# Kernel tuning notes

Hardware: AMD Instinct MI355X
Metric: run time of the kernel (lower is better)

## Reference

```python
import jax, jax.numpy as jnp
import numpy as np

K = 100
TEMPERATURE = 0.1


def setup_inputs() -> dict:
    key = jax.random.key(0)
    k1, k2 = jax.random.split(key)
    x = jax.random.normal(k1, (8, 128, 60, 60), dtype=jnp.float32)
    W = jax.random.normal(k2, (128, 2 * K), dtype=jnp.float32) * 0.02  # torch Linear(k*2, d_model).weight
    b = jnp.zeros((128,), dtype=jnp.float32)
    return {"x": x, "W": W, "b": b}


def reference(x, W, b):
    x0, x1 = jnp.split(x, 2, axis=0)
    n, c, h, w = x0.shape
    hw = h * w
    # n c h w -> n (h w) c
    f0 = jnp.transpose(x0.reshape(n, c, hw), (0, 2, 1))
    f1 = jnp.transpose(x1.reshape(n, c, hw), (0, 2, 1))
    # (f0/sqrt(c)) @ (f1/sqrt(c))^T / T  ==  f0 @ f1^T / (c*T)
    sm = jnp.einsum('nld,nsd->nls', f0, f1) / (c * TEMPERATURE)
    cm = (jax.nn.softmax(sm, axis=1) * jax.nn.softmax(sm, axis=2)).reshape(n, hw * hw)
    _, topi = jax.lax.top_k(cm, K)  # (n, K)
    qindex = topi // hw
    rindex = topi % hw
    coords0 = jnp.stack([qindex % w, qindex // w], axis=-1).astype(jnp.float32) / w  # (n, K, 2) as (x, y)
    coords1 = jnp.stack([rindex % w, rindex // w], axis=-1).astype(jnp.float32) / w
    # create_meshgrid(h, w, normalized=False): (1, h*w, 2) with (x, y), row-major
    gy, gx = jnp.meshgrid(jnp.arange(h), jnp.arange(w), indexing='ij')
    grid = jnp.stack([gx, gy], axis=-1).reshape(1, hw, 2).astype(jnp.float32) / w
    offsets0 = grid[:, :, None, :] - coords0[:, None, :, :]  # (n, hw, K, 2)
    offsets1 = grid[:, :, None, :] - coords1[:, None, :, :]
    emb0 = offsets0.reshape(n, hw, 2 * K) @ W.T + b  # (n, hw, d_model)
    emb1 = offsets1.reshape(n, hw, 2 * K) @ W.T + b
    f0 = f0 + emb0
    f1 = f1 + emb1
    f = jnp.concatenate([f0, f1], axis=0)  # (2n, hw, d)
    # n (h w) d -> n d h w
    return jnp.transpose(f, (0, 2, 1)).reshape(2 * n, c, h, w)
```

## Files before the change

kernel.cpp:

```cpp
#include <hip/hip_runtime.h>

#define HW 3600
#define PADR 3712
#define NF4 900
#define CAP 16384
#define KSEL 100
#define NT 58
typedef unsigned long long U64;

using short8   = __attribute__((ext_vector_type(8))) short;
using float4v  = __attribute__((ext_vector_type(4))) float;
using float16v = __attribute__((ext_vector_type(16))) float;

__device__ __forceinline__ unsigned monof(float f) {
    unsigned b = __float_as_uint(f);
    return (b & 0x80000000u) ? ~b : (b | 0x80000000u);
}
__device__ __forceinline__ float unmonof(unsigned m) {
    return __uint_as_float((m & 0x80000000u) ? (m ^ 0x80000000u) : ~m);
}
__device__ __forceinline__ unsigned short f2bf(float f) {
    unsigned b = __float_as_uint(f);
    return (unsigned short)((b + 0x7FFFu + ((b >> 16) & 1u)) >> 16);
}
__device__ __forceinline__ float bf2f(unsigned short h) {
    return __uint_as_float(((unsigned)h) << 16);
}
__device__ __forceinline__ void async16(const void* g, void* l) {
    __builtin_amdgcn_global_load_lds((const __attribute__((address_space(1))) void*)g,
                                     (__attribute__((address_space(3))) void*)l, 16, 0, 0);
}


__global__ __launch_bounds__(256) void conv_k(
    const float* __restrict__ x,
    unsigned short* __restrict__ hiT, unsigned short* __restrict__ loT,
    unsigned* __restrict__ zero_region)
{
    int b = blockIdx.z, l0 = blockIdx.x * 64, d0 = blockIdx.y * 64;
    __shared__ float t[64][65];
    int tid = threadIdx.x;
    if (blockIdx.y == 0 && blockIdx.z == 0) {
        int base = blockIdx.x * 512;
        for (int i = tid; i < 512; i += 256) {
            int g = base + i;
            if (g < 28808) zero_region[g] = 0u;
        }
    }
#pragma unroll
    for (int r = 0; r < 4; r++) {
        int idx = tid + 256 * r;
        int d = idx >> 4, lq = idx & 15;
        int l = l0 + lq * 4;
        const float* src = x + ((size_t)b * 128 + d0 + d) * HW;
        float4 v;
        if (l + 3 < HW) v = *(const float4*)(src + l);
        else {
            v.x = (l     < HW) ? src[l]     : 0.f;
            v.y = (l + 1 < HW) ? src[l + 1] : 0.f;
            v.z = (l + 2 < HW) ? src[l + 2] : 0.f;
            v.w = (l + 3 < HW) ? src[l + 3] : 0.f;
        }
        t[lq * 4 + 0][d] = v.x; t[lq * 4 + 1][d] = v.y;
        t[lq * 4 + 2][d] = v.z; t[lq * 4 + 3][d] = v.w;
    }
    __syncthreads();
    const int rblk = l0 >> 7;
#pragma unroll
    for (int r = 0; r < 2; r++) {
        int idx = tid + 256 * r;
        int l = idx & 63, dq = idx >> 6;
        unsigned hp[4], lp[4];
#pragma unroll
        for (int j = 0; j < 4; j++) {
            float f0 = t[l][dq * 8 + 2 * j], f1 = t[l][dq * 8 + 2 * j + 1];
            unsigned short h0 = f2bf(f0), h1 = f2bf(f1);
            unsigned short g0 = f2bf(f0 - bf2f(h0)), g1 = f2bf(f1 - bf2f(h1));
            hp[j] = (unsigned)h0 | ((unsigned)h1 << 16);
            lp[j] = (unsigned)g0 | ((unsigned)g1 << 16);
        }
        size_t o = ((size_t)(b * 29 + rblk) * 16 + (d0 >> 3) + dq) * 1024
                 + (size_t)((l0 + l) & 127) * 8;
        *(uint4*)(hiT + o) = make_uint4(hp[0], hp[1], hp[2], hp[3]);
        *(uint4*)(loT + o) = make_uint4(lp[0], lp[1], lp[2], lp[3]);
    }
}

__global__ __launch_bounds__(512) void gemm_mfma_k(
    const unsigned short* __restrict__ hiT, const unsigned short* __restrict__ loT,
    float* __restrict__ den_row, float* __restrict__ den_col,
    float* __restrict__ maxvt)
{
    const int batch = blockIdx.z, bx = blockIdx.x, by = blockIdx.y;
    __shared__ __align__(16) union SU {
        unsigned short st[4][4][128][8];
        float T[8192];
    } u;
    __shared__ float rsB[128];
    __shared__ float csB[128];
    __shared__ unsigned mxB[2][128];

    const int tid = threadIdx.x;
    const int lane = tid & 63, w = tid >> 6;
    const int l31 = lane & 31, h = lane >> 5;
    const int p = w >> 1, halfr = w & 1;
    const int rg = w >> 2, cg = w & 3;

    if (tid < 128) { rsB[tid] = 0.f; csB[tid] = 0.f; }
    if (tid < 256) mxB[tid >> 7][tid & 127] = 0u;

    const unsigned short* psrc = (p == 0) ? hiT : (p == 1) ? loT : (p == 2) ? hiT : loT;
    const int bsel = (p < 2) ? batch : batch + 4;
    const int rblk = (p < 2) ? by : bx;
    const size_t cbase = ((size_t)(bsel * 29 + rblk) * 16) * 1024;

    float16v acc[2];
    acc[0] = (float16v)(0.f);
    acc[1] = (float16v)(0.f);

    for (int k0 = 0; k0 < 128; k0 += 32) {
#pragma unroll
        for (int kb = 0; kb < 4; kb++) {
            const unsigned short* g = psrc + cbase + (size_t)((k0 >> 3) + kb) * 1024
                                    + (halfr << 9) + lane * 8;
            async16(g, &u.st[p][kb][halfr << 6][0]);
        }
        __syncthreads();
#pragma unroll
        for (int j = 0; j < 2; j++) {
            int kb = j * 2 + h;
            short8 ah[2], al[2], bh, bl;
            ah[0] = *(const short8*)&u.st[0][kb][rg * 64 + l31][0];
            ah[1] = *(const short8*)&u.st[0][kb][rg * 64 + 32 + l31][0];
            al[0] = *(const short8*)&u.st[1][kb][rg * 64 + l31][0];
            al[1] = *(const short8*)&u.st[1][kb][rg * 64 + 32 + l31][0];
            bh    = *(const short8*)&u.st[2][kb][cg * 32 + l31][0];
            bl    = *(const short8*)&u.st[3][kb][cg * 32 + l31][0];
#pragma unroll
            for (int mt = 0; mt < 2; mt++) {
                acc[mt] = __builtin_amdgcn_mfma_f32_32x32x16_bf16(ah[mt], bh, acc[mt], 0, 0, 0);
                acc[mt] = __builtin_amdgcn_mfma_f32_32x32x16_bf16(ah[mt], bl, acc[mt], 0, 0, 0);
                acc[mt] = __builtin_amdgcn_mfma_f32_32x32x16_bf16(al[mt], bh, acc[mt], 0, 0, 0);
            }
        }
        __syncthreads();
    }

    const float scale = 0.078125f;
    float* T = u.T + w * 1024;
    const bool interior = (bx < 28) && (by < 28);
    const int col0 = bx * 128 + cg * 32 + l31;
    const bool cv = interior || (col0 < HW);
    float cs = 0.f;

#pragma unroll
    for (int mt = 0; mt < 2; mt++) {
#pragma unroll
        for (int reg = 0; reg < 16; reg++) {
            float v = acc[mt][reg] * scale;
            float e = cv ? __expf(v) : 0.f;
            int rloc = (reg & 3) + 8 * (reg >> 2) + 4 * h;
            bool rv = interior || (by * 128 + rg * 64 + mt * 32 + rloc < HW);
            if (rv) cs += e;
            T[rloc * 32 + (l31 ^ rloc)] = e;
        }
        __asm__ __volatile__("s_waitcnt lgkmcnt(0)" ::: "memory");
        {
            float ps = 0.f, pm = 0.f;
#pragma unroll
            for (int i = 0; i < 16; i++) {
                float tv_ = T[l31 * 32 + ((h * 16 + i) ^ l31)];
                ps += tv_;
                pm = fmaxf(pm, tv_);
            }
            ps += __shfl_xor(ps, 32);
            pm = fmaxf(pm, __shfl_xor(pm, 32));
            if (h == 0) {
                atomicAdd(&rsB[rg * 64 + mt * 32 + l31], ps);
                atomicMax(&mxB[cg >> 1][rg * 64 + mt * 32 + l31],
                          monof(__logf(pm)));
            }
        }
        __asm__ __volatile__("s_waitcnt lgkmcnt(0)" ::: "memory");
    }
    cs += __shfl_xor(cs, 32);
    if (h == 0) atomicAdd(&csB[cg * 32 + l31], cs);
    __syncthreads();

    if (tid < 128) {
        int l = by * 128 + tid;
        if (l < HW) atomicAdd(&den_row[(size_t)batch * HW + l], rsB[tid]);
        int s = bx * 128 + tid;
        if (s < HW) atomicAdd(&den_col[(size_t)batch * HW + s], csB[tid]);
    }
    if (tid < 256) {
        int tile = tid >> 7, row = tid & 127;
        int l = by * 128 + row;
        if (l < HW)
            maxvt[((size_t)batch * NT + bx * 2 + tile) * PADR + l] =
                unmonof(mxB[tile][row]);
    }
}

__global__ __launch_bounds__(256) void stat_k(
    const float* __restrict__ den_row, const float* __restrict__ den_col,
    const float* __restrict__ maxvt, float* __restrict__ keylb)
{
    const int b = blockIdx.z, tid = threadIdx.x;
    __shared__ float lncS[HW];
    __shared__ float mlsS[NT];
    for (int i = tid; i < HW; i += 256)
        lncS[i] = __logf(den_col[(size_t)b * HW + i]);
    __syncthreads();
    if (tid < NT) {
        float mx = -3.4e38f;
        int s0 = tid * 64, s1 = s0 + 64; if (s1 > HW) s1 = HW;
        for (int s = s0; s < s1; s++) mx = fmaxf(mx, lncS[s]);
        mlsS[tid] = (s0 < HW) ? mx : 1e30f;
    }
    __syncthreads();
    int j = blockIdx.x * 240 + tid;
    if (tid < 240 && j < HW) {
        const float* mvb = maxvt + (size_t)b * NT * PADR;
        float b0 = -3.4e38f, b1_ = -3.4e38f;
#pragma unroll 4
        for (int tt = 0; tt < 58; tt += 2) {
            b0  = fmaxf(b0,  2.0f * mvb[(size_t)tt * PADR + j]       - mlsS[tt]);
            b1_ = fmaxf(b1_, 2.0f * mvb[(size_t)(tt + 1) * PADR + j] - mlsS[tt + 1]);
        }
        keylb[(size_t)b * HW + j] = fmaxf(b0, b1_) - __logf(den_row[(size_t)b * HW + j]);
    }
}

__global__ __launch_bounds__(256) void tau_k(
    const float* __restrict__ keylb, float* __restrict__ tau)
{
    const int b = blockIdx.z, tid = threadIdx.x;
    __shared__ unsigned keyS[HW];
    __shared__ unsigned hist[4096];
    __shared__ unsigned hpc[256];
    __shared__ int b1S, c1S, b2S, lcnt;
    __shared__ unsigned bestS;
    __shared__ unsigned list[1024];

    for (int i = tid; i < 4096; i += 256) hist[i] = 0u;
    if (tid == 0) { lcnt = 0; bestS = 0u; }
    __syncthreads();
    for (int i = tid; i < HW; i += 256) {
        unsigned k = monof(keylb[(size_t)b * HW + i]);
        keyS[i] = k;
        atomicAdd(&hist[k >> 20], 1u);
    }
    __syncthreads();
    { unsigned s = 0; for (int j = 0; j < 16; j++) s += hist[tid * 16 + j]; hpc[tid] = s; }
    __syncthreads();
    if (tid == 0) {
        unsigned cum = 0; int cs_ = 255;
        for (; cs_ > 0; cs_--) { if (cum + hpc[cs_] >= (unsigned)KSEL) break; cum += hpc[cs_]; }
        int bb = cs_ * 16 + 15;
        for (; bb > cs_ * 16; bb--) { if (cum + hist[bb] >= (unsigned)KSEL) break; cum += hist[bb]; }
        b1S = bb; c1S = (int)cum;
    }
    __syncthreads();
    int b1 = b1S;
    for (int i = tid; i < 4096; i += 256) hist[i] = 0u;
    __syncthreads();
    for (int i = tid; i < HW; i += 256) {
        unsigned k = keyS[i];
        if ((int)(k >> 20) == b1) atomicAdd(&hist[(k >> 8) & 4095], 1u);
    }
    __syncthreads();
    { unsigned s = 0; for (int j = 0; j < 16; j++) s += hist[tid * 16 + j]; hpc[tid] = s; }
    __syncthreads();
    if (tid == 0) {
        unsigned cum = (unsigned)c1S; int cs_ = 255;
        for (; cs_ > 0; cs_--) { if (cum + hpc[cs_] >= (unsigned)KSEL) break; cum += hpc[cs_]; }
        int bb = cs_ * 16 + 15;
        for (; bb > cs_ * 16; bb--) { if (cum + hist[bb] >= (unsigned)KSEL) break; cum += hist[bb]; }
        b2S = bb;
    }
    __syncthreads();
    int b2 = b2S;
    for (int i = tid; i < HW; i += 256) {
        unsigned k = keyS[i]; int hb = (int)(k >> 20);
        if (hb > b1 || (hb == b1 && (int)((k >> 8) & 4095) >= b2)) {
            int p = atomicAdd(&lcnt, 1);
            if (p < 1024) list[p] = k;
        }
    }
    __syncthreads();
    int L = lcnt; if (L > 1024) L = 1024;
    for (int i = tid; i < L; i += 256) {
        unsigned e = list[i]; int c = 0;
        for (int j = 0; j < L; j++) c += (list[j] >= e) ? 1 : 0;
        if (c >= KSEL) atomicMax(&bestS, e);
    }
    __syncthreads();
    if (tid == 0) tau[b] = unmonof(bestS) - 3e-4f;
}

__global__ __launch_bounds__(256) void recollect_k(
    const unsigned short* __restrict__ hiT, const unsigned short* __restrict__ loT,
    const float* __restrict__ den_row, const float* __restrict__ den_col,
    const float* __restrict__ maxvt, const float* __restrict__ tau,
    uint2* __restrict__ cand, int* __restrict__ cnt)
{
    const int t = blockIdx.x, batch = blockIdx.y;
    const int tid = threadIdx.x;
    __shared__ float lnrS[HW];
    __shared__ float lncS[64];
    __shared__ int prS[2048];
    __shared__ int pcS;
    __shared__ float mnlS;
    __shared__ __align__(16) unsigned short bS[2][16][64][8];

    const int lane = tid & 63, w = tid >> 6;
    const size_t bbase = (size_t)(batch + 4) * PADR * 128;

    {
        const size_t sbase = bbase + (size_t)(t >> 1) * 16 * 1024
                           + (size_t)(t & 1) * 512 + (size_t)lane * 8;
#pragma unroll
        for (int s = w; s < 32; s += 4) {
            const int buf = s >> 4, kb = s & 15;
            const unsigned short* g = (buf ? loT : hiT) + sbase + (size_t)kb * 1024;
            async16(g, &bS[buf][kb][0][0]);
        }
    }

    if (tid < 64) {
        int c = t * 64 + tid;
        float lc = (c < HW) ? __logf(den_col[(size_t)batch * HW + c]) : 1e30f;
        lncS[tid] = lc;
        float mn = lc;
#pragma unroll
        for (int off = 1; off < 64; off <<= 1) mn = fminf(mn, __shfl_xor(mn, off));
        if (tid == 0) mnlS = mn;
    }
    for (int r = tid; r < HW; r += 256)
        lnrS[r] = __logf(den_row[(size_t)batch * HW + r]);
    if (tid == 0) pcS = 0;
    __syncthreads();

    const float tv = tau[batch];
    const float tvm = tv - 3e-4f;
    const float mnl = mnlS;
    const float* mv = maxvt + ((size_t)batch * NT + t) * PADR;
    for (int r = tid; r < HW; r += 256) {
        float bnd = 2.0f * mv[r] - lnrS[r] - mnl;
        if (bnd >= tvm) {
            int p = atomicAdd(&pcS, 1);
            if (p < 2048) prS[p] = r;
        }
    }
    __syncthreads();
    int pc = pcS; if (pc > 2048) pc = 2048;
    if (pc == 0) return;

    const int m = lane & 15, q = lane >> 4;
    const float scale = 0.078125f;
    const size_t abase = (size_t)batch * PADR * 128;

    for (int g = w; g * 16 < pc; g += 4) {
        int pi = g * 16 + m;
        int rowv = (pi < pc) ? prS[pi] : HW;
        float ldrv = (pi < pc) ? lnrS[rowv] : 0.f;
        size_t arow = abase + ((size_t)(rowv >> 7) * 16) * 1024 + (size_t)(rowv & 127) * 8;

        float4v acc[4];
#pragma unroll
        for (int i = 0; i < 4; i++) acc[i] = (float4v){0.f, 0.f, 0.f, 0.f};
#pragma unroll
        for (int k0 = 0; k0 < 128; k0 += 32) {
            int kb = (k0 >> 3) + q;
            short8 ah = *(const short8*)(hiT + arow + (size_t)kb * 1024);
            short8 al = *(const short8*)(loT + arow + (size_t)kb * 1024);
#pragma unroll
            for (int nt = 0; nt < 4; nt++) {
                short8 bh = *(const short8*)&bS[0][kb][nt * 16 + m][0];
                short8 bl = *(const short8*)&bS[1][kb][nt * 16 + m][0];
                acc[nt] = __builtin_amdgcn_mfma_f32_16x16x32_bf16(ah, bh, acc[nt], 0, 0, 0);
                acc[nt] = __builtin_amdgcn_mfma_f32_16x16x32_bf16(ah, bl, acc[nt], 0, 0, 0);
                acc[nt] = __builtin_amdgcn_mfma_f32_16x16x32_bf16(al, bh, acc[nt], 0, 0, 0);
            }
        }
#pragma unroll
        for (int nt = 0; nt < 4; nt++) {
            int c = t * 64 + nt * 16 + m;
            if (c >= HW) continue;
            float ldc = lncS[nt * 16 + m];
#pragma unroll
            for (int r = 0; r < 4; r++) {
                int ri = q * 4 + r;
                if (g * 16 + ri >= pc) continue;
                int rowo = __shfl(rowv, ri);
                float ldro = __shfl(ldrv, ri);
                float v = acc[nt][r] * scale;
                float tt2 = 2.0f * v - ldro - ldc;
                if (tt2 >= tv) {
                    int p = atomicAdd(&cnt[batch], 1);
                    if (p < CAP)
                        cand[(size_t)batch * CAP + p] =
                            make_uint2(monof(tt2), (unsigned)(rowo * HW + c));
                }
            }
        }
    }
}

__global__ __launch_bounds__(1024) void select_k(
    const uint2* __restrict__ cand, const int* __restrict__ cnt,
    const float* __restrict__ W, const float* __restrict__ bias,
    float* __restrict__ cst, float* __restrict__ sxy)
{
    const int batch = blockIdx.x;
    const int tid = threadIdx.x;
    const uint2* cb = cand + (size_t)batch * CAP;
    __shared__ U64 lk[6144];
    __shared__ int topiS[KSEL];
    __shared__ float cqx[KSEL], cqy[KSEL], crx[KSEL], cry[KSEL];

    int M = cnt[batch]; if (M > CAP) M = CAP;
    const bool useL = (M <= 6144);
    if (useL)
        for (int i = tid; i < M; i += 1024) {
            uint2 e = cb[i];
            lk[i] = ((U64)e.x << 32) | (unsigned)(~e.y);
        }
    __syncthreads();
    for (int i = tid; i < M; i += 1024) {
        U64 e;
        if (useL) e = lk[i];
        else { uint2 tt = cb[i]; e = ((U64)tt.x << 32) | (unsigned)(~tt.y); }
        int r = 0;
        for (int j = 0; j < M; j++) {
            U64 o;
            if (useL) o = lk[j];
            else { uint2 tt = cb[j]; o = ((U64)tt.x << 32) | (unsigned)(~tt.y); }
            r += (o > e) ? 1 : 0;
        }
        if (r < KSEL) topiS[r] = (int)(~(unsigned)(e & 0xffffffffu));
    }
    __syncthreads();
    if (tid < KSEL) {
        int idx = topiS[tid];
        int qq = idx / HW, rr = idx - qq * HW;
        cqx[tid] = (float)(qq % 60) / 60.0f;
        cqy[tid] = (float)(qq / 60) / 60.0f;
        crx[tid] = (float)(rr % 60) / 60.0f;
        cry[tid] = (float)(rr / 60) / 60.0f;
    }
    __syncthreads();
    if (tid < 256) {
        const int d = tid & 127, hf = tid >> 7;
        const float* wrow = W + d * 200;
        float sx = 0.f, sy = 0.f, c = 0.f;
#pragma unroll 4
        for (int k = 0; k < KSEL; k++) {
            float wx = wrow[2 * k], wy = wrow[2 * k + 1];
            sx += wx; sy += wy;
            float cx = hf ? crx[k] : cqx[k];
            float cy = hf ? cry[k] : cqy[k];
            c += cx * wx + cy * wy;
        }
        cst[(hf ? (batch + 4) : batch) * 128 + d] = bias[d] - c;
        if (batch == 0 && hf == 0) { sxy[d] = sx; sxy[128 + d] = sy; }
    }
}

__global__ __launch_bounds__(256) void final_k(
    const float* __restrict__ x, const float* __restrict__ cst,
    const float* __restrict__ sxy, float* __restrict__ out)
{
    const int bd = blockIdx.x;
    const int d = bd & 127;
    const int tid = threadIdx.x;
    const float cstv = cst[bd];
    const float sx = sxy[d], sy = sxy[128 + d];
    const float4* xin = (const float4*)(x + (size_t)bd * HW);
    float4* o4 = (float4*)(out + (size_t)bd * HW);
    for (int f = tid; f < NF4; f += 256) {
        float4 v = xin[f];
        int p0 = f * 4;
        float gy = (float)(p0 / 60) / 60.0f;
        float gxb = (float)(p0 % 60);
        float add = cstv + gy * sy;
        v.x += add + ((gxb      ) / 60.0f) * sx;
        v.y += add + ((gxb + 1.f) / 60.0f) * sx;
        v.z += add + ((gxb + 2.f) / 60.0f) * sx;
        v.w += add + ((gxb + 3.f) / 60.0f) * sx;
        o4[f] = v;
    }
}

extern "C" void kernel_launch(void* const* d_in, const int* in_sizes, int n_in,
                              void* d_out, int out_size, void* d_ws, size_t ws_size,
                              hipStream_t stream)
{
    const float* x    = (const float*)d_in[0];
    const float* W    = (const float*)d_in[1];
    const float* bias = (const float*)d_in[2];
    float* out = (float*)d_out;

    char* ws = (char*)d_ws;
    float*    den_row = (float*)(ws + 0);
    float*    den_col = (float*)(ws + 57600);
    int*      cnt     = (int*)  (ws + 115200);
    float*    tau     = (float*)(ws + 115216);
    float*    keylb   = (float*)(ws + 115264);
    float*    cst     = (float*)(ws + 115264);
    float*    sxy     = (float*)(ws + 119360);
    uint2*    cand    = (uint2*)(ws + 172864);
    float*    maxvt   = (float*)(ws + 697152);
    unsigned short* hiT = (unsigned short*)(ws + 4141888);
    unsigned short* loT = (unsigned short*)(ws + 11744064);

    conv_k     <<<dim3(58, 2, 8),  256, 0, stream>>>(x, hiT, loT, (unsigned*)ws);
    gemm_mfma_k<<<dim3(29, 29, 4), 512, 0, stream>>>(hiT, loT, den_row, den_col, maxvt);
    stat_k     <<<dim3(15, 1, 4),  256, 0, stream>>>(den_row, den_col, maxvt, keylb);
    tau_k      <<<dim3(1, 1, 4),   256, 0, stream>>>(keylb, tau);
    recollect_k<<<dim3(NT, 4),     256, 0, stream>>>(hiT, loT, den_row, den_col, maxvt, tau, cand, cnt);
    select_k   <<<dim3(4),         1024, 0, stream>>>(cand, cnt, W, bias, cst, sxy);
    final_k    <<<dim3(1024),      256, 0, stream>>>(x, cst, sxy, out);
}
```

Before: 224.6 us.

## Use 4 waves with 2x2 MFMA tiles per wave in similarity GEMM

The similarity GEMM block drops from 8 waves to 4. Each wave now computes a 64x64 sub-tile (2x2 of 32x32 MFMA tiles) instead of 64x32, so each LDS fragment it loads is reused across more MFMAs. Each wave also issues twice as many async loads to stage its operand slab. The epilogue is reworked to match, at the cost of more accumulator registers per thread and less latency hiding per block.

```diff
diff --git a/kernel.cpp b/kernel.cpp
--- a/kernel.cpp
+++ b/kernel.cpp
@@ -86,7 +86,7 @@
     }
 }
 
-__global__ __launch_bounds__(512) void gemm_mfma_k(
+__global__ __launch_bounds__(256) void gemm_mfma_k(
     const unsigned short* __restrict__ hiT, const unsigned short* __restrict__ loT,
     float* __restrict__ den_row, float* __restrict__ den_col,
     float* __restrict__ maxvt)
@@ -94,7 +94,7 @@
     const int batch = blockIdx.z, bx = blockIdx.x, by = blockIdx.y;
     __shared__ __align__(16) union SU {
         unsigned short st[4][4][128][8];
-        float T[8192];
+        float T[4096];
     } u;
     __shared__ float rsB[128];
     __shared__ float csB[128];
@@ -103,44 +103,51 @@
     const int tid = threadIdx.x;
     const int lane = tid & 63, w = tid >> 6;
     const int l31 = lane & 31, h = lane >> 5;
-    const int p = w >> 1, halfr = w & 1;
-    const int rg = w >> 2, cg = w & 3;
+    const int rw = (w >> 1) * 64, cw = (w & 1) * 64;
 
     if (tid < 128) { rsB[tid] = 0.f; csB[tid] = 0.f; }
-    if (tid < 256) mxB[tid >> 7][tid & 127] = 0u;
-
-    const unsigned short* psrc = (p == 0) ? hiT : (p == 1) ? loT : (p == 2) ? hiT : loT;
-    const int bsel = (p < 2) ? batch : batch + 4;
-    const int rblk = (p < 2) ? by : bx;
+    mxB[tid >> 7][tid & 127] = 0u;
+
+    const unsigned short* psrc = (w == 0) ? hiT : (w == 1) ? loT : (w == 2) ? hiT : loT;
+    const int bsel = (w < 2) ? batch : batch + 4;
+    const int rblk = (w < 2) ? by : bx;
     const size_t cbase = ((size_t)(bsel * 29 + rblk) * 16) * 1024;
 
-    float16v acc[2];
-    acc[0] = (float16v)(0.f);
-    acc[1] = (float16v)(0.f);
+    float16v acc[4];
+#pragma unroll
+    for (int i = 0; i < 4; i++) acc[i] = (float16v)(0.f);
 
     for (int k0 = 0; k0 < 128; k0 += 32) {
 #pragma unroll
         for (int kb = 0; kb < 4; kb++) {
-            const unsigned short* g = psrc + cbase + (size_t)((k0 >> 3) + kb) * 1024
-                                    + (halfr << 9) + lane * 8;
-            async16(g, &u.st[p][kb][halfr << 6][0]);
+#pragma unroll
+            for (int hr = 0; hr < 2; hr++) {
+                const unsigned short* g = psrc + cbase + (size_t)((k0 >> 3) + kb) * 1024
+                                        + (hr << 9) + lane * 8;
+                async16(g, &u.st[w][kb][hr << 6][0]);
+            }
         }
         __syncthreads();
 #pragma unroll
         for (int j = 0; j < 2; j++) {
             int kb = j * 2 + h;
-            short8 ah[2], al[2], bh, bl;
-            ah[0] = *(const short8*)&u.st[0][kb][rg * 64 + l31][0];
-            ah[1] = *(const short8*)&u.st[0][kb][rg * 64 + 32 + l31][0];
-            al[0] = *(const short8*)&u.st[1][kb][rg * 64 + l31][0];
-            al[1] = *(const short8*)&u.st[1][kb][rg * 64 + 32 + l31][0];
-            bh    = *(const short8*)&u.st[2][kb][cg * 32 + l31][0];
-            bl    = *(const short8*)&u.st[3][kb][cg * 32 + l31][0];
-#pragma unroll
-            for (int mt = 0; mt < 2; mt++) {
-                acc[mt] = __builtin_amdgcn_mfma_f32_32x32x16_bf16(ah[mt], bh, acc[mt], 0, 0, 0);
-                acc[mt] = __builtin_amdgcn_mfma_f32_32x32x16_bf16(ah[mt], bl, acc[mt], 0, 0, 0);
-                acc[mt] = __builtin_amdgcn_mfma_f32_32x32x16_bf16(al[mt], bh, acc[mt], 0, 0, 0);
+            short8 ah[2], al[2], bh[2], bl[2];
+#pragma unroll
+            for (int i = 0; i < 2; i++) {
+                ah[i] = *(const short8*)&u.st[0][kb][rw + i * 32 + l31][0];
+                al[i] = *(const short8*)&u.st[1][kb][rw + i * 32 + l31][0];
+                bh[i] = *(const short8*)&u.st[2][kb][cw + i * 32 + l31][0];
+                bl[i] = *(const short8*)&u.st[3][kb][cw + i * 32 + l31][0];
+            }
+#pragma unroll
+            for (int mr = 0; mr < 2; mr++) {
+#pragma unroll
+                for (int mc = 0; mc < 2; mc++) {
+                    const int a = mr * 2 + mc;
+                    acc[a] = __builtin_amdgcn_mfma_f32_32x32x16_bf16(ah[mr], bh[mc], acc[a], 0, 0, 0);
+                    acc[a] = __builtin_amdgcn_mfma_f32_32x32x16_bf16(ah[mr], bl[mc], acc[a], 0, 0, 0);
+                    acc[a] = __builtin_amdgcn_mfma_f32_32x32x16_bf16(al[mr], bh[mc], acc[a], 0, 0, 0);
+                }
             }
         }
         __syncthreads();
@@ -149,42 +156,51 @@
     const float scale = 0.078125f;
     float* T = u.T + w * 1024;
     const bool interior = (bx < 28) && (by < 28);
-    const int col0 = bx * 128 + cg * 32 + l31;
-    const bool cv = interior || (col0 < HW);
-    float cs = 0.f;
-
-#pragma unroll
-    for (int mt = 0; mt < 2; mt++) {
-#pragma unroll
-        for (int reg = 0; reg < 16; reg++) {
-            float v = acc[mt][reg] * scale;
-            float e = cv ? __expf(v) : 0.f;
-            int rloc = (reg & 3) + 8 * (reg >> 2) + 4 * h;
-            bool rv = interior || (by * 128 + rg * 64 + mt * 32 + rloc < HW);
-            if (rv) cs += e;
-            T[rloc * 32 + (l31 ^ rloc)] = e;
-        }
-        __asm__ __volatile__("s_waitcnt lgkmcnt(0)" ::: "memory");
-        {
-            float ps = 0.f, pm = 0.f;
-#pragma unroll
-            for (int i = 0; i < 16; i++) {
-                float tv_ = T[l31 * 32 + ((h * 16 + i) ^ l31)];
-                ps += tv_;
-                pm = fmaxf(pm, tv_);
-            }
-            ps += __shfl_xor(ps, 32);
-            pm = fmaxf(pm, __shfl_xor(pm, 32));
-            if (h == 0) {
-                atomicAdd(&rsB[rg * 64 + mt * 32 + l31], ps);
-                atomicMax(&mxB[cg >> 1][rg * 64 + mt * 32 + l31],
-                          monof(__logf(pm)));
-            }
-        }
-        __asm__ __volatile__("s_waitcnt lgkmcnt(0)" ::: "memory");
-    }
-    cs += __shfl_xor(cs, 32);
-    if (h == 0) atomicAdd(&csB[cg * 32 + l31], cs);
+    float csa[2] = {0.f, 0.f};
+
+#pragma unroll
+    for (int mr = 0; mr < 2; mr++) {
+#pragma unroll
+        for (int mc = 0; mc < 2; mc++) {
+            const int a = mr * 2 + mc;
+            const int col0 = bx * 128 + cw + mc * 32 + l31;
+            const bool cv = interior || (col0 < HW);
+            float cpart = 0.f;
+#pragma unroll
+            for (int reg = 0; reg < 16; reg++) {
+                float v = acc[a][reg] * scale;
+                float e = cv ? __expf(v) : 0.f;
+                int rloc = (reg & 3) + 8 * (reg >> 2) + 4 * h;
+                bool rv = interior || (by * 128 + rw + mr * 32 + rloc < HW);
+                if (rv) cpart += e;
+                T[rloc * 32 + (l31 ^ rloc)] = e;
+            }
+            __asm__ __volatile__("s_waitcnt lgkmcnt(0)" ::: "memory");
+            {
+                float ps = 0.f, pm = 0.f;
+#pragma unroll
+                for (int i = 0; i < 16; i++) {
+                    float tv_ = T[l31 * 32 + ((h * 16 + i) ^ l31)];
+                    ps += tv_;
+                    pm = fmaxf(pm, tv_);
+                }
+                ps += __shfl_xor(ps, 32);
+                pm = fmaxf(pm, __shfl_xor(pm, 32));
+                if (h == 0) {
+                    atomicAdd(&rsB[rw + mr * 32 + l31], ps);
+                    atomicMax(&mxB[w & 1][rw + mr * 32 + l31],
+                              monof(__logf(pm)));
+                }
+            }
+            __asm__ __volatile__("s_waitcnt lgkmcnt(0)" ::: "memory");
+            csa[mc] += cpart;
+        }
+    }
+#pragma unroll
+    for (int mc = 0; mc < 2; mc++) {
+        float c2 = csa[mc] + __shfl_xor(csa[mc], 32);
+        if (h == 0) atomicAdd(&csB[cw + mc * 32 + l31], c2);
+    }
     __syncthreads();
 
     if (tid < 128) {
@@ -193,7 +209,7 @@
         int s = bx * 128 + tid;
         if (s < HW) atomicAdd(&den_col[(size_t)batch * HW + s], csB[tid]);
     }
-    if (tid < 256) {
+    {
         int tile = tid >> 7, row = tid & 127;
         int l = by * 128 + row;
         if (l < HW)
@@ -516,7 +532,7 @@
     unsigned short* loT = (unsigned short*)(ws + 11744064);
 
     conv_k     <<<dim3(58, 2, 8),  256, 0, stream>>>(x, hiT, loT, (unsigned*)ws);
-    gemm_mfma_k<<<dim3(29, 29, 4), 512, 0, stream>>>(hiT, loT, den_row, den_col, maxvt);
+    gemm_mfma_k<<<dim3(29, 29, 4), 256, 0, stream>>>(hiT, loT, den_row, den_col, maxvt);
     stat_k     <<<dim3(15, 1, 4),  256, 0, stream>>>(den_row, den_col, maxvt, keylb);
     tau_k      <<<dim3(1, 1, 4),   256, 0, stream>>>(keylb, tau);
     recollect_k<<<dim3(NT, 4),     256, 0, stream>>>(hiT, loT, den_row, den_col, maxvt, tau, cand, cnt);
```

Result: no change. 226.7 us (+0.9%).
